# Performance work log

Hardware: AMD Instinct MI355X
Metric: run time of the kernel (lower is better)

The kernel has to match this reference:

```python
import jax, jax.numpy as jnp
import numpy as np


def _conv3d(x, w):
    # x: [N, C, D, H, W], w: [O, I, K, K, K] -> [N, O, D', H', W'] VALID conv
    return jax.lax.conv_general_dilated(
        x, w, window_strides=(1, 1, 1), padding='VALID',
        dimension_numbers=('NCDHW', 'OIDHW', 'NCDHW'))


def conv4d(x, w):
    # x: [B, C, D1, D2, D3, D4]; w: [O, I, K1, K2, K3, K4]
    # Decompose 4D conv as a sum over K1 taps of 3D convs; the sliced D1
    # window is folded into the batch dimension so XLA's 3D conv does the work.
    B, C, D1, D2, D3, D4 = x.shape
    O, I, K1, K2, K3, K4 = w.shape
    D1o = D1 - K1 + 1
    out = None
    for i in range(K1):  # small fixed loop over kernel taps (K1=3)
        xs = jax.lax.dynamic_slice_in_dim(x, i, D1o, axis=2)      # [B,C,D1o,D2,D3,D4]
        xs = xs.transpose(0, 2, 1, 3, 4, 5).reshape(B * D1o, C, D2, D3, D4)
        y = _conv3d(xs, w[:, :, i])                                # [B*D1o,O,d2,d3,d4]
        out = y if out is None else out + y
    d2, d3, d4 = out.shape[2], out.shape[3], out.shape[4]
    out = out.reshape(B, D1o, O, d2, d3, d4).transpose(0, 2, 1, 3, 4, 5)
    return out  # [B, O, D1o, d2, d3, d4]


def setup_inputs() -> dict:
    key = jax.random.key(0)
    k1, k2 = jax.random.split(key)
    pic_in = jax.random.normal(k1, (2, 16, 8, 8, 64, 64), dtype=jnp.float32)
    # convNd weight: [out_channels, in_channels, K, K, K, K], no bias
    weight = jax.random.normal(k2, (32, 16, 3, 3, 3, 3), dtype=jnp.float32) * 0.05
    return {"pic_in": pic_in, "weight": weight}


def reference(pic_in, weight):
    # ConvKernel.forward: 4D conv (stride 1, padding 0, no bias) + ReLU
    return jax.nn.relu(conv4d(pic_in, weight))
```

## Files before the change

kernel.cpp:

```cpp
#include <hip/hip_runtime.h>


typedef __attribute__((ext_vector_type(8))) __bf16 bf16x8;
typedef __attribute__((ext_vector_type(16))) float f32x16;

#define CSTRIDE 262144

#define WT_OFF 0
#define XB_OFF 131072
#define BOFF 16640
#define BUF 25856

typedef __attribute__((address_space(1))) const unsigned int gu32;
typedef __attribute__((address_space(3))) unsigned int lu32;

__device__ __forceinline__ void async_cp16(const void* g, void* l) {
  __builtin_amdgcn_global_load_lds((gu32*)g, (lu32*)l, 16, 0, 0);
}

__global__ __launch_bounds__(256) void prep(const float* __restrict__ x,
                                            const float* __restrict__ w,
                                            unsigned char* __restrict__ ws) {
  int blk = blockIdx.x;
  if (blk < 2048) {
    __bf16* xb = (__bf16*)(ws + XB_OFF);
    int n = blk * 256 + threadIdx.x;
    int col = n & 63;
    int d3 = (n >> 6) & 63;
    int d2 = (n >> 12) & 7;
    int d1 = (n >> 15) & 7;
    int b = n >> 18;
    const float* gx =
        x + ((((size_t)(b * 16) * 8 + d1) * 8 + d2) * 64 + d3) * 64 + col;
    float v[16];
#pragma unroll
    for (int c = 0; c < 16; ++c) v[c] = gx[(size_t)c * CSTRIDE];
    __bf16* row = xb + ((((b * 8 + d1) * 8 + d2) * 64 + d3) * 1024);
#pragma unroll
    for (int ch = 0; ch < 2; ++ch) {
      bf16x8 o;
#pragma unroll
      for (int cc = 0; cc < 8; ++cc) o[cc] = (__bf16)v[ch * 8 + cc];
      *(bf16x8*)(row + ch * 512 + col * 8) = o;
    }
  } else {
    int o = blk - 2048;
    __bf16* wT = (__bf16*)(ws + WT_OFF);
#pragma unroll
    for (int base = 0; base < 1296; base += 256) {
      int idx = base + threadIdx.x;
      if (idx < 1296) {
        int c = idx / 81, t = idx % 81;
        wT[t * 512 + o * 16 + c] = (__bf16)w[o * 1296 + idx];
      }
    }
  }
}

template <int NT>
__device__ __forceinline__ void conv_body(
    const unsigned char* __restrict__ wTb, const unsigned char* __restrict__ xbb,
    float* __restrict__ out, unsigned char* lds, int b, int e1, int e2,
    int r0) {
  int lane = threadIdx.x & 63;
  int wave = threadIdx.x >> 6;
  int m32 = lane & 31;
  int half = lane >> 5;
  int rg = wave >> 1;
  int th = wave & 1;
  int rowbase = rg * NT;
  const int nckA = (NT * 2 + 2) * 2;

  int ab_off = half * 1024 + (th * 32 + m32) * 16;
  int bb_off = m32 * 32 + half * 16;

  f32x16 acc[NT];
#pragma unroll
  for (int i = 0; i < NT; ++i)
#pragma unroll
    for (int r = 0; r < 16; ++r) acc[i][r] = 0.f;

  {
    const unsigned char* gA =
        xbb + (size_t)(((b * 8 + e1) * 8 + e2) * 64 + r0) * 2048;
#pragma unroll
    for (int j = 0; j < 4; ++j) {
      int ck = j * 4 + wave;
      if (ck < nckA) async_cp16(gA + ck * 1024 + lane * 16, lds + ck * 1024);
    }
#pragma unroll
    for (int j = 0; j < 3; ++j) {
      int ck = j * 4 + wave;
      if (ck < 9)
        async_cp16(wTb + ck * 1024 + lane * 16, lds + BOFF + ck * 1024);
    }
  }

  for (int p = 0; p < 9; ++p) {
    __syncthreads();
    if (p < 8) {
      int np = p + 1;
      int nk1 = np / 3, nk2 = np - nk1 * 3;
      const unsigned char* gA =
          xbb + (size_t)(((b * 8 + e1 + nk1) * 8 + e2 + nk2) * 64 + r0) * 2048;
      const unsigned char* gB = wTb + np * 9216;
      unsigned char* dst = lds + (np & 1) * BUF;
#pragma unroll
      for (int j = 0; j < 4; ++j) {
        int ck = j * 4 + wave;
        if (ck < nckA) async_cp16(gA + ck * 1024 + lane * 16, dst + ck * 1024);
      }
#pragma unroll
      for (int j = 0; j < 3; ++j) {
        int ck = j * 4 + wave;
        if (ck < 9)
          async_cp16(gB + ck * 1024 + lane * 16, dst + BOFF + ck * 1024);
      }
    }
    const unsigned char* bufp = lds + (p & 1) * BUF;
    bf16x8 bfr[9];
#pragma unroll
    for (int t9 = 0; t9 < 9; ++t9)
      bfr[t9] = *(const bf16x8*)(bufp + BOFF + t9 * 1024 + bb_off);
    const unsigned char* abase = bufp + rowbase * 2048 + ab_off;
    __builtin_amdgcn_s_setprio(1);
#pragma unroll
    for (int k4 = 0; k4 < 3; ++k4) {
      bf16x8 arow[NT + 2];
#pragma unroll
      for (int j = 0; j < NT + 2; ++j)
        arow[j] = *(const bf16x8*)(abase + j * 2048 + k4 * 16);
#pragma unroll
      for (int k3 = 0; k3 < 3; ++k3) {
        bf16x8 bf = bfr[k3 * 3 + k4];
#pragma unroll
        for (int i = 0; i < NT; ++i)
          acc[i] = __builtin_amdgcn_mfma_f32_32x32x16_bf16(arow[i + k3], bf,
                                                           acc[i], 0, 0, 0);
      }
    }
    __builtin_amdgcn_s_setprio(0);
  }
  __syncthreads();

  float* sc = (float*)(void*)lds + wave * 1056;
  int e4 = th * 32 + m32;
#pragma unroll
  for (int i = 0; i < NT; ++i) {
    int e3 = r0 + rowbase + i;
#pragma unroll
    for (int r = 0; r < 16; ++r) {
      int m = (r & 3) + 8 * (r >> 2) + 4 * half;
      sc[m * 33 + m32] = acc[i][r];
    }
    size_t obase =
        ((((size_t)b * 32) * 6 + e1) * 6 + e2) * 3844 + (size_t)e3 * 62;
#pragma unroll
    for (int it = 0; it < 16; ++it) {
      int o = it * 2 + half;
      float v = fmaxf(sc[m32 * 33 + o], 0.f);
      if (e4 < 62) out[obase + (size_t)o * 138384 + e4] = v;
    }
  }
}

__global__ __launch_bounds__(256, 3) void conv_mfma(
    const unsigned char* __restrict__ ws, float* __restrict__ out) {
  const unsigned char* wTb = ws + WT_OFF;
  const unsigned char* xbb = ws + XB_OFF;

  __shared__ __align__(16) unsigned char lds[2 * BUF];

  int bid = blockIdx.x;
  int g = bid % 72;
  int chunk = bid / 72;
  int b = g / 36;
  int e1 = (g / 6) % 6;
  int e2 = g % 6;
  int r0 = chunk * 6;

  if (chunk < 10)
    conv_body<3>(wTb, xbb, out, lds, b, e1, e2, r0);
  else
    conv_body<1>(wTb, xbb, out, lds, b, e1, e2, r0);
}

extern "C" void kernel_launch(void* const* d_in, const int* in_sizes, int n_in,
                              void* d_out, int out_size, void* d_ws,
                              size_t ws_size, hipStream_t stream) {
  const float* x = (const float*)d_in[0];
  const float* w = (const float*)d_in[1];
  float* out = (float*)d_out;
  unsigned char* ws = (unsigned char*)d_ws;
  prep<<<dim3(2080), dim3(256), 0, stream>>>(x, w, ws);
  conv_mfma<<<dim3(792), dim3(256), 0, stream>>>(ws, out);
}
```

Measured before the change: 111.0 us.

## Use 2-wave blocks with each wave computing all six output rows

The conv block shrinks from 4 waves to 2. Each wave now covers a 32-column half and all R rows, not a 3-row by half split. This raises A-fragment reuse per wave, since R+2 row loads feed 3R MFMAs instead of NT+2 feeding 3NT. The async-copy loops are merged so two waves share the input and weight staging. The cost is a larger accumulator set per wave (6 f32x16), fewer waves per block and lower occupancy (launch bounds 128,2), which may expose more latency.

After: 114.8 us. 1.03x slower.

```diff
diff --git a/kernel.cpp b/kernel.cpp
--- a/kernel.cpp
+++ b/kernel.cpp
@@ -57,7 +57,7 @@
   }
 }
 
-template <int NT>
+template <int R>
 __device__ __forceinline__ void conv_body(
     const unsigned char* __restrict__ wTb, const unsigned char* __restrict__ xbb,
     float* __restrict__ out, unsigned char* lds, int b, int e1, int e2,
@@ -66,17 +66,16 @@
   int wave = threadIdx.x >> 6;
   int m32 = lane & 31;
   int half = lane >> 5;
-  int rg = wave >> 1;
-  int th = wave & 1;
-  int rowbase = rg * NT;
-  const int nckA = (NT * 2 + 2) * 2;
+  const int nckA = (R + 2) * 2;
+  const int nck = nckA + 9;
+  const int jmax = (nck + 1) / 2;
 
-  int ab_off = half * 1024 + (th * 32 + m32) * 16;
+  int ab_off = half * 1024 + (wave * 32 + m32) * 16;
   int bb_off = m32 * 32 + half * 16;
 
-  f32x16 acc[NT];
+  f32x16 acc[R];
 #pragma unroll
-  for (int i = 0; i < NT; ++i)
+  for (int i = 0; i < R; ++i)
 #pragma unroll
     for (int r = 0; r < 16; ++r) acc[i][r] = 0.f;
 
@@ -84,15 +83,13 @@
     const unsigned char* gA =
         xbb + (size_t)(((b * 8 + e1) * 8 + e2) * 64 + r0) * 2048;
 #pragma unroll
-    for (int j = 0; j < 4; ++j) {
-      int ck = j * 4 + wave;
-      if (ck < nckA) async_cp16(gA + ck * 1024 + lane * 16, lds + ck * 1024);
-    }
-#pragma unroll
-    for (int j = 0; j < 3; ++j) {
-      int ck = j * 4 + wave;
-      if (ck < 9)
-        async_cp16(wTb + ck * 1024 + lane * 16, lds + BOFF + ck * 1024);
+    for (int j = 0; j < jmax; ++j) {
+      int ck = j * 2 + wave;
+      if (ck < nckA)
+        async_cp16(gA + ck * 1024 + lane * 16, lds + ck * 1024);
+      else if (ck < nck)
+        async_cp16(wTb + (ck - nckA) * 1024 + lane * 16,
+                   lds + BOFF + (ck - nckA) * 1024);
     }
   }
 
@@ -106,15 +103,13 @@
       const unsigned char* gB = wTb + np * 9216;
       unsigned char* dst = lds + (np & 1) * BUF;
 #pragma unroll
-      for (int j = 0; j < 4; ++j) {
-        int ck = j * 4 + wave;
-        if (ck < nckA) async_cp16(gA + ck * 1024 + lane * 16, dst + ck * 1024);
-      }
-#pragma unroll
-      for (int j = 0; j < 3; ++j) {
-        int ck = j * 4 + wave;
-        if (ck < 9)
-          async_cp16(gB + ck * 1024 + lane * 16, dst + BOFF + ck * 1024);
+      for (int j = 0; j < jmax; ++j) {
+        int ck = j * 2 + wave;
+        if (ck < nckA)
+          async_cp16(gA + ck * 1024 + lane * 16, dst + ck * 1024);
+        else if (ck < nck)
+          async_cp16(gB + (ck - nckA) * 1024 + lane * 16,
+                     dst + BOFF + (ck - nckA) * 1024);
       }
     }
     const unsigned char* bufp = lds + (p & 1) * BUF;
@@ -122,19 +117,19 @@
 #pragma unroll
     for (int t9 = 0; t9 < 9; ++t9)
       bfr[t9] = *(const bf16x8*)(bufp + BOFF + t9 * 1024 + bb_off);
-    const unsigned char* abase = bufp + rowbase * 2048 + ab_off;
+    const unsigned char* abase = bufp + ab_off;
     __builtin_amdgcn_s_setprio(1);
 #pragma unroll
     for (int k4 = 0; k4 < 3; ++k4) {
-      bf16x8 arow[NT + 2];
+      bf16x8 arow[R + 2];
 #pragma unroll
-      for (int j = 0; j < NT + 2; ++j)
+      for (int j = 0; j < R + 2; ++j)
         arow[j] = *(const bf16x8*)(abase + j * 2048 + k4 * 16);
 #pragma unroll
       for (int k3 = 0; k3 < 3; ++k3) {
         bf16x8 bf = bfr[k3 * 3 + k4];
 #pragma unroll
-        for (int i = 0; i < NT; ++i)
+        for (int i = 0; i < R; ++i)
           acc[i] = __builtin_amdgcn_mfma_f32_32x32x16_bf16(arow[i + k3], bf,
                                                            acc[i], 0, 0, 0);
       }
@@ -144,10 +139,10 @@
   __syncthreads();
 
   float* sc = (float*)(void*)lds + wave * 1056;
-  int e4 = th * 32 + m32;
+  int e4 = wave * 32 + m32;
 #pragma unroll
-  for (int i = 0; i < NT; ++i) {
-    int e3 = r0 + rowbase + i;
+  for (int i = 0; i < R; ++i) {
+    int e3 = r0 + i;
 #pragma unroll
     for (int r = 0; r < 16; ++r) {
       int m = (r & 3) + 8 * (r >> 2) + 4 * half;
@@ -164,7 +159,7 @@
   }
 }
 
-__global__ __launch_bounds__(256, 3) void conv_mfma(
+__global__ __launch_bounds__(128, 2) void conv_mfma(
     const unsigned char* __restrict__ ws, float* __restrict__ out) {
   const unsigned char* wTb = ws + WT_OFF;
   const unsigned char* xbb = ws + XB_OFF;
@@ -180,9 +175,9 @@
   int r0 = chunk * 6;
 
   if (chunk < 10)
-    conv_body<3>(wTb, xbb, out, lds, b, e1, e2, r0);
+    conv_body<6>(wTb, xbb, out, lds, b, e1, e2, r0);
   else
-    conv_body<1>(wTb, xbb, out, lds, b, e1, e2, r0);
+    conv_body<2>(wTb, xbb, out, lds, b, e1, e2, r0);
 }
 
 extern "C" void kernel_launch(void* const* d_in, const int* in_sizes, int n_in,
@@ -193,5 +188,5 @@
   float* out = (float*)d_out;
   unsigned char* ws = (unsigned char*)d_ws;
   prep<<<dim3(2080), dim3(256), 0, stream>>>(x, w, ws);
-  conv_mfma<<<dim3(792), dim3(256), 0, stream>>>(ws, out);
+  conv_mfma<<<dim3(792), dim3(128), 0, stream>>>(ws, out);
 }
```

## Fuse prep and conv into one cooperative persistent kernel with grid sync

Applied to the files above, without the earlier changes.

Replaces the two-launch sequence (bf16 prep/transposition, then MFMA conv) with a single cooperative kernel of 768 blocks. The blocks loop over the prep units, do a grid-wide sync, then loop over the 792 conv units, falling back to the two launches if the cooperative launch fails. The async load loops for the A and B tiles are also merged into one loop so the waves share the copy work more evenly. This is meant to remove the second launch and the gap between kernels, at the cost of a grid barrier, 24 conv units left over for a second pass, and an extra __syncthreads per unit.

Result: slower. 244.0 us (+119.8%).

```diff
diff --git a/kernel.cpp b/kernel.cpp
--- a/kernel.cpp
+++ b/kernel.cpp
@@ -1,4 +1,5 @@
 #include <hip/hip_runtime.h>
+#include <hip/hip_cooperative_groups.h>
 
 
 typedef __attribute__((ext_vector_type(8))) __bf16 bf16x8;
@@ -18,13 +19,12 @@
   __builtin_amdgcn_global_load_lds((gu32*)g, (lu32*)l, 16, 0, 0);
 }
 
-__global__ __launch_bounds__(256) void prep(const float* __restrict__ x,
-                                            const float* __restrict__ w,
-                                            unsigned char* __restrict__ ws) {
-  int blk = blockIdx.x;
-  if (blk < 2048) {
+__device__ __forceinline__ void prep_unit(int vb, const float* __restrict__ x,
+                                          const float* __restrict__ w,
+                                          unsigned char* __restrict__ ws) {
+  if (vb < 2048) {
     __bf16* xb = (__bf16*)(ws + XB_OFF);
-    int n = blk * 256 + threadIdx.x;
+    int n = vb * 256 + threadIdx.x;
     int col = n & 63;
     int d3 = (n >> 6) & 63;
     int d2 = (n >> 12) & 7;
@@ -44,7 +44,7 @@
       *(bf16x8*)(row + ch * 512 + col * 8) = o;
     }
   } else {
-    int o = blk - 2048;
+    int o = vb - 2048;
     __bf16* wT = (__bf16*)(ws + WT_OFF);
 #pragma unroll
     for (int base = 0; base < 1296; base += 256) {
@@ -55,6 +55,12 @@
       }
     }
   }
+}
+
+__global__ __launch_bounds__(256) void prep(const float* __restrict__ x,
+                                            const float* __restrict__ w,
+                                            unsigned char* __restrict__ ws) {
+  prep_unit(blockIdx.x, x, w, ws);
 }
 
 template <int NT>
@@ -70,6 +76,7 @@
   int th = wave & 1;
   int rowbase = rg * NT;
   const int nckA = (NT * 2 + 2) * 2;
+  const int nck = nckA + 9;
 
   int ab_off = half * 1024 + (th * 32 + m32) * 16;
   int bb_off = m32 * 32 + half * 16;
@@ -84,15 +91,13 @@
     const unsigned char* gA =
         xbb + (size_t)(((b * 8 + e1) * 8 + e2) * 64 + r0) * 2048;
 #pragma unroll
-    for (int j = 0; j < 4; ++j) {
+    for (int j = 0; j < 7; ++j) {
       int ck = j * 4 + wave;
-      if (ck < nckA) async_cp16(gA + ck * 1024 + lane * 16, lds + ck * 1024);
-    }
-#pragma unroll
-    for (int j = 0; j < 3; ++j) {
-      int ck = j * 4 + wave;
-      if (ck < 9)
-        async_cp16(wTb + ck * 1024 + lane * 16, lds + BOFF + ck * 1024);
+      if (ck < nckA)
+        async_cp16(gA + ck * 1024 + lane * 16, lds + ck * 1024);
+      else if (ck < nck)
+        async_cp16(wTb + (ck - nckA) * 1024 + lane * 16,
+                   lds + BOFF + (ck - nckA) * 1024);
     }
   }
 
@@ -106,15 +111,13 @@
       const unsigned char* gB = wTb + np * 9216;
       unsigned char* dst = lds + (np & 1) * BUF;
 #pragma unroll
-      for (int j = 0; j < 4; ++j) {
+      for (int j = 0; j < 7; ++j) {
         int ck = j * 4 + wave;
-        if (ck < nckA) async_cp16(gA + ck * 1024 + lane * 16, dst + ck * 1024);
-      }
-#pragma unroll
-      for (int j = 0; j < 3; ++j) {
-        int ck = j * 4 + wave;
-        if (ck < 9)
-          async_cp16(gB + ck * 1024 + lane * 16, dst + BOFF + ck * 1024);
+        if (ck < nckA)
+          async_cp16(gA + ck * 1024 + lane * 16, dst + ck * 1024);
+        else if (ck < nck)
+          async_cp16(gB + (ck - nckA) * 1024 + lane * 16,
+                     dst + BOFF + (ck - nckA) * 1024);
       }
     }
     const unsigned char* bufp = lds + (p & 1) * BUF;
@@ -162,27 +165,42 @@
       if (e4 < 62) out[obase + (size_t)o * 138384 + e4] = v;
     }
   }
-}
-
-__global__ __launch_bounds__(256, 3) void conv_mfma(
-    const unsigned char* __restrict__ ws, float* __restrict__ out) {
+  __syncthreads();
+}
+
+__device__ __forceinline__ void conv_unit(int unit,
+                                          const unsigned char* __restrict__ ws,
+                                          float* __restrict__ out,
+                                          unsigned char* lds) {
   const unsigned char* wTb = ws + WT_OFF;
   const unsigned char* xbb = ws + XB_OFF;
-
-  __shared__ __align__(16) unsigned char lds[2 * BUF];
-
-  int bid = blockIdx.x;
-  int g = bid % 72;
-  int chunk = bid / 72;
+  int g = unit % 72;
+  int chunk = unit / 72;
   int b = g / 36;
   int e1 = (g / 6) % 6;
   int e2 = g % 6;
   int r0 = chunk * 6;
-
   if (chunk < 10)
     conv_body<3>(wTb, xbb, out, lds, b, e1, e2, r0);
   else
     conv_body<1>(wTb, xbb, out, lds, b, e1, e2, r0);
+}
+
+__global__ __launch_bounds__(256, 3) void conv_mfma(
+    const unsigned char* __restrict__ ws, float* __restrict__ out) {
+  __shared__ __align__(16) unsigned char lds[2 * BUF];
+  conv_unit(blockIdx.x, ws, out, lds);
+}
+
+__global__ __launch_bounds__(256, 3) void fused(const float* __restrict__ x,
+                                                const float* __restrict__ w,
+                                                unsigned char* __restrict__ ws,
+                                                float* __restrict__ out) {
+  __shared__ __align__(16) unsigned char lds[2 * BUF];
+  int bid = blockIdx.x;
+  for (int vb = bid; vb < 2080; vb += 768) prep_unit(vb, x, w, ws);
+  cooperative_groups::this_grid().sync();
+  for (int unit = bid; unit < 792; unit += 768) conv_unit(unit, ws, out, lds);
 }
 
 extern "C" void kernel_launch(void* const* d_in, const int* in_sizes, int n_in,
@@ -192,6 +210,12 @@
   const float* w = (const float*)d_in[1];
   float* out = (float*)d_out;
   unsigned char* ws = (unsigned char*)d_ws;
-  prep<<<dim3(2080), dim3(256), 0, stream>>>(x, w, ws);
-  conv_mfma<<<dim3(792), dim3(256), 0, stream>>>(ws, out);
-}
+
+  void* args[] = {(void*)&x, (void*)&w, (void*)&ws, (void*)&out};
+  hipError_t e = hipLaunchCooperativeKernel((const void*)fused, dim3(768),
+                                            dim3(256), args, 0, stream);
+  if (e != hipSuccess) {
+    prep<<<dim3(2080), dim3(256), 0, stream>>>(x, w, ws);
+    conv_mfma<<<dim3(792), dim3(256), 0, stream>>>(ws, out);
+  }
+}
```

## Split weight layout by channel halves, balance async copies, and schedule tail chunk first

Applied to the files above, without the earlier changes.

Reorders the bf16 weight tensor so each 8-channel half of every tap occupies a contiguous 512-byte region. The B-fragment LDS reads then become lane-contiguous 16-byte loads instead of a 32-byte stride, which is meant to reduce LDS bank conflicts. The A and B async-copy loops are merged into one chunk index so the copy work spreads evenly over the waves. Block-to-chunk mapping is rotated so the small NT=1 tail blocks launch first, which changes the tail-effect scheduling.

Result: no change. 112.1 us (+1.0%).

```diff
diff --git a/kernel.cpp b/kernel.cpp
--- a/kernel.cpp
+++ b/kernel.cpp
@@ -51,7 +51,8 @@
       int idx = base + threadIdx.x;
       if (idx < 1296) {
         int c = idx / 81, t = idx % 81;
-        wT[t * 512 + o * 16 + c] = (__bf16)w[o * 1296 + idx];
+        wT[t * 512 + (c >> 3) * 256 + o * 8 + (c & 7)] =
+            (__bf16)w[o * 1296 + idx];
       }
     }
   }
@@ -70,9 +71,10 @@
   int th = wave & 1;
   int rowbase = rg * NT;
   const int nckA = (NT * 2 + 2) * 2;
+  const int nck = nckA + 9;
 
   int ab_off = half * 1024 + (th * 32 + m32) * 16;
-  int bb_off = m32 * 32 + half * 16;
+  int bb_off = half * 512 + m32 * 16;
 
   f32x16 acc[NT];
 #pragma unroll
@@ -84,15 +86,13 @@
     const unsigned char* gA =
         xbb + (size_t)(((b * 8 + e1) * 8 + e2) * 64 + r0) * 2048;
 #pragma unroll
-    for (int j = 0; j < 4; ++j) {
+    for (int j = 0; j < 7; ++j) {
       int ck = j * 4 + wave;
-      if (ck < nckA) async_cp16(gA + ck * 1024 + lane * 16, lds + ck * 1024);
-    }
-#pragma unroll
-    for (int j = 0; j < 3; ++j) {
-      int ck = j * 4 + wave;
-      if (ck < 9)
-        async_cp16(wTb + ck * 1024 + lane * 16, lds + BOFF + ck * 1024);
+      if (ck < nckA)
+        async_cp16(gA + ck * 1024 + lane * 16, lds + ck * 1024);
+      else if (ck < nck)
+        async_cp16(wTb + (ck - nckA) * 1024 + lane * 16,
+                   lds + BOFF + (ck - nckA) * 1024);
     }
   }
 
@@ -106,15 +106,13 @@
       const unsigned char* gB = wTb + np * 9216;
       unsigned char* dst = lds + (np & 1) * BUF;
 #pragma unroll
-      for (int j = 0; j < 4; ++j) {
+      for (int j = 0; j < 7; ++j) {
         int ck = j * 4 + wave;
-        if (ck < nckA) async_cp16(gA + ck * 1024 + lane * 16, dst + ck * 1024);
-      }
-#pragma unroll
-      for (int j = 0; j < 3; ++j) {
-        int ck = j * 4 + wave;
-        if (ck < 9)
-          async_cp16(gB + ck * 1024 + lane * 16, dst + BOFF + ck * 1024);
+        if (ck < nckA)
+          async_cp16(gA + ck * 1024 + lane * 16, dst + ck * 1024);
+        else if (ck < nck)
+          async_cp16(gB + (ck - nckA) * 1024 + lane * 16,
+                     dst + BOFF + (ck - nckA) * 1024);
       }
     }
     const unsigned char* bufp = lds + (p & 1) * BUF;
@@ -173,7 +171,7 @@
 
   int bid = blockIdx.x;
   int g = bid % 72;
-  int chunk = bid / 72;
+  int chunk = (bid / 72 + 10) % 11;
   int b = g / 36;
   int e1 = (g / 6) % 6;
   int e2 = g % 6;
```
